# Kernel tuning notes

Hardware: AMD Instinct MI355X
Metric: run time of the kernel (lower is better)

The kernel has to match this reference:

```python
import jax, jax.numpy as jnp
import numpy as np

T, B, E = 2048, 2, 256
H = 8
D = E // H


def setup_inputs() -> dict:
    key = jax.random.key(0)
    ks = jax.random.split(key, 10)
    s = 1.0 / np.sqrt(E)
    return {
        "query": jax.random.normal(ks[0], (T, B, E), jnp.float32),
        "attn_bias": jax.random.normal(ks[1], (B, T, T), jnp.float32),
        "Wq": jax.random.normal(ks[2], (E, E), jnp.float32) * s,
        "bq": jax.random.normal(ks[3], (E,), jnp.float32) * 0.02,
        "Wk": jax.random.normal(ks[4], (E, E), jnp.float32) * s,
        "bk": jax.random.normal(ks[5], (E,), jnp.float32) * 0.02,
        "Wv": jax.random.normal(ks[6], (E, E), jnp.float32) * s,
        "bv": jax.random.normal(ks[7], (E,), jnp.float32) * 0.02,
        "Wo": jax.random.normal(ks[8], (E, E), jnp.float32) * s,
        "bo": jax.random.normal(ks[9], (E,), jnp.float32) * 0.02,
    }


def reference(query, attn_bias, Wq, bq, Wk, bk, Wv, bv, Wo, bo):
    # query: [T, B, E] (seq-first). Self-attention: k,v also projected from query.
    t, b, e = query.shape
    scaling = 1.0 / np.sqrt(D)
    q = (query @ Wq.T + bq) * scaling          # [T,B,E]
    k = query @ Wk.T + bk                      # [T,B,E]
    v = query @ Wv.T + bv                      # [T,B,E]
    q = q.reshape(t, b, H, D)
    k = k.reshape(t, b, H, D)
    v = v.reshape(t, b, H, D)
    # raw scores + per-batch additive bias broadcast across heads
    scores = jnp.einsum("tbhd,sbhd->bhts", q, k) + attn_bias[:, None, :, :]
    attn_weights = jax.nn.softmax(scores, axis=-1)  # [B,H,T,S]
    attn = jnp.einsum("bhts,sbhd->tbhd", attn_weights, v).reshape(t, b, e)
    return attn @ Wo.T + bo  # [T,B,E]
```

## Files before the change

kernel.cpp:

```cpp
#include <hip/hip_runtime.h>
#include <hip/hip_bf16.h>

#define T_DIM 2048
#define B_DIM 2
#define E_DIM 256
#define H_DIM 8
#define D_DIM 32
#define M_DIM (T_DIM*B_DIM)
#define SPLIT 4
#define S_CHUNK (T_DIM/SPLIT)
#define BHT (B_DIM*H_DIM*T_DIM)

typedef __bf16 bf16x8 __attribute__((ext_vector_type(8)));
typedef __bf16 bf16x4 __attribute__((ext_vector_type(4)));
typedef __bf16 bf16x2 __attribute__((ext_vector_type(2)));
typedef float  f32x4  __attribute__((ext_vector_type(4)));

static __device__ __forceinline__ float fexp2(float x) {
#if __has_builtin(__builtin_amdgcn_exp2f)
    return __builtin_amdgcn_exp2f(x);
#else
    return exp2f(x);
#endif
}

__global__ __launch_bounds__(256)
void qkv_kernel(const float* __restrict__ X,
                const float* __restrict__ Wq, const float* __restrict__ Wk, const float* __restrict__ Wv,
                const float* __restrict__ bq, const float* __restrict__ bk, const float* __restrict__ bv,
                __bf16* __restrict__ qh, __bf16* __restrict__ kperm, __bf16* __restrict__ vperm) {
    __shared__ __align__(16) __bf16 Xs[64][136];
    __shared__ __align__(16) __bf16 Ws[64][136];
    const int m0 = blockIdx.x * 64;
    const int which = blockIdx.y >> 2;
    const int n0 = (blockIdx.y & 3) * 64;
    const float* W = (which == 0) ? Wq : (which == 1) ? Wk : Wv;
    const float* bias = (which == 0) ? bq : (which == 1) ? bk : bv;
    const int tid = threadIdx.x;
    const int wid = tid >> 6, lane = tid & 63;
    const int wm = (wid & 1) * 32, wn = (wid >> 1) * 32;
    const int lr = lane & 15, lg = lane >> 4;

    f32x4 acc[2][2] = {};
    for (int kc = 0; kc < 2; ++kc) {
        for (int c = tid; c < 2048; c += 256) {
            int row = c >> 5, col = (c & 31) * 4;
            float4 xv = *(const float4*)&X[(size_t)(m0 + row) * E_DIM + kc * 128 + col];
            float4 wv = *(const float4*)&W[(size_t)(n0 + row) * E_DIM + kc * 128 + col];
            bf16x4 xb, wb;
            xb[0] = (__bf16)xv.x; xb[1] = (__bf16)xv.y; xb[2] = (__bf16)xv.z; xb[3] = (__bf16)xv.w;
            wb[0] = (__bf16)wv.x; wb[1] = (__bf16)wv.y; wb[2] = (__bf16)wv.z; wb[3] = (__bf16)wv.w;
            *(bf16x4*)&Xs[row][col] = xb;
            *(bf16x4*)&Ws[row][col] = wb;
        }
        __syncthreads();
#pragma unroll
        for (int ks = 0; ks < 4; ++ks) {
            bf16x8 a0 = *(const bf16x8*)&Xs[wm + lr][ks * 32 + lg * 8];
            bf16x8 a1 = *(const bf16x8*)&Xs[wm + 16 + lr][ks * 32 + lg * 8];
            bf16x8 b0 = *(const bf16x8*)&Ws[wn + lr][ks * 32 + lg * 8];
            bf16x8 b1 = *(const bf16x8*)&Ws[wn + 16 + lr][ks * 32 + lg * 8];
            acc[0][0] = __builtin_amdgcn_mfma_f32_16x16x32_bf16(a0, b0, acc[0][0], 0, 0, 0);
            acc[0][1] = __builtin_amdgcn_mfma_f32_16x16x32_bf16(a0, b1, acc[0][1], 0, 0, 0);
            acc[1][0] = __builtin_amdgcn_mfma_f32_16x16x32_bf16(a1, b0, acc[1][0], 0, 0, 0);
            acc[1][1] = __builtin_amdgcn_mfma_f32_16x16x32_bf16(a1, b1, acc[1][1], 0, 0, 0);
        }
        __syncthreads();
    }
    const float scale = 0.17677669529663687f * 1.4426950408889634f;
#pragma unroll
    for (int mt = 0; mt < 2; ++mt) {
#pragma unroll
        for (int nt = 0; nt < 2; ++nt) {
            int n = n0 + wn + nt * 16 + lr;
            float bb = bias[n];
            int h = n >> 5, d = n & 31;
#pragma unroll
            for (int r = 0; r < 4; ++r) {
                int m = m0 + wm + mt * 16 + lg * 4 + r;
                int t = m >> 1, b = m & 1;
                float v = acc[mt][nt][r] + bb;
                if (which == 0) {
                    v *= scale;
                    qh[((size_t)(b * H_DIM + h) * T_DIM + t) * D_DIM + d] = (__bf16)v;
                } else if (which == 1) {
                    int til = t >> 6, s6 = t & 63;
                    int ntk = ((s6 >> 5) << 1) | ((s6 >> 2) & 1);
                    int lrk = (((s6 >> 3) & 3) << 2) | (s6 & 3);
                    int lanek = ((d >> 3) << 4) | lrk;
                    kperm[((((size_t)(b * H_DIM + h) * 32 + til) * 4 + ntk) * 64 + lanek) * 8 + (d & 7)] = (__bf16)v;
                } else {
                    int til = t >> 6;
                    int ktv = (t >> 5) & 1, lgv = (t >> 3) & 3, elv = t & 7;
                    int jv = ktv * 2 + (d >> 4);
                    int lanev = (lgv << 4) | (d & 15);
                    vperm[((((size_t)(b * H_DIM + h) * 32 + til) * 4 + jv) * 64 + lanev) * 8 + elv] = (__bf16)v;
                }
            }
        }
    }
}

__global__ __launch_bounds__(512, 4)
void attn_kernel(const __bf16* __restrict__ qh, const __bf16* __restrict__ kperm,
                 const __bf16* __restrict__ vperm, const float* __restrict__ attn_bias,
                 __bf16* __restrict__ po, float* __restrict__ pl) {
    __shared__ __align__(16) float Bs[16][516];
    const int lin = blockIdx.x + (T_DIM / 16) * (blockIdx.y + B_DIM * blockIdx.z);
    const int combo = lin & 7;
    const int b  = combo & 1;
    const int sp = combo >> 1;
    const int t0 = (lin >> 3) * 16;
    const int tid = threadIdx.x, wid = tid >> 6, lane = tid & 63;
    const int lr = lane & 15, lg = lane >> 4;
    const int bh = b * H_DIM + wid;
    const int sbase = sp * S_CHUNK;
    const int tb0 = sp * 8;
    const float LOG2E = 1.4426950408889634f;

    {
        const float* bsrc = attn_bias + ((size_t)b * T_DIM + t0) * T_DIM + sbase;
        int r = tid >> 5, c0 = (tid & 31) * 4;
#pragma unroll
        for (int rep = 0; rep < 4; ++rep) {
            float4 v = *(const float4*)&bsrc[(size_t)r * T_DIM + rep * 128 + c0];
            float4 w;
            w.x = (v.x - 12.0f) * LOG2E;
            w.y = (v.y - 12.0f) * LOG2E;
            w.z = (v.z - 12.0f) * LOG2E;
            w.w = (v.w - 12.0f) * LOG2E;
            *(float4*)&Bs[r][rep * 128 + c0] = w;
        }
    }
    __syncthreads();

    bf16x8 qf = *(const bf16x8*)&qh[((size_t)bh * T_DIM + t0 + lr) * D_DIM + lg * 8];
    const __bf16* kpb = kperm + (size_t)bh * T_DIM * D_DIM + (size_t)lane * 8;
    const __bf16* vpb = vperm + (size_t)bh * T_DIM * D_DIM + (size_t)lane * 8;

    bf16x8 ones;
#pragma unroll
    for (int i = 0; i < 8; ++i) ones[i] = (__bf16)1.0f;

    f32x4 o0 = {}, o1 = {};
    f32x4 ol = {};

#pragma unroll
    for (int st = 0; st < 8; ++st) {
        const int til = tb0 + st;

        bf16x8 kf0 = *(const bf16x8*)&kpb[(size_t)(til * 4 + 0) * 512];
        bf16x8 kf1 = *(const bf16x8*)&kpb[(size_t)(til * 4 + 1) * 512];
        bf16x8 kf2 = *(const bf16x8*)&kpb[(size_t)(til * 4 + 2) * 512];
        bf16x8 kf3 = *(const bf16x8*)&kpb[(size_t)(til * 4 + 3) * 512];
        bf16x8 vf0 = *(const bf16x8*)&vpb[(size_t)(til * 4 + 0) * 512];
        bf16x8 vf1 = *(const bf16x8*)&vpb[(size_t)(til * 4 + 1) * 512];
        bf16x8 vf2 = *(const bf16x8*)&vpb[(size_t)(til * 4 + 2) * 512];
        bf16x8 vf3 = *(const bf16x8*)&vpb[(size_t)(til * 4 + 3) * 512];

        f32x4 cb0 = *(const f32x4*)&Bs[lr][st * 64 +  0 + lg * 8 + 0];
        f32x4 cb1 = *(const f32x4*)&Bs[lr][st * 64 +  0 + lg * 8 + 4];
        f32x4 cb2 = *(const f32x4*)&Bs[lr][st * 64 + 32 + lg * 8 + 0];
        f32x4 cb3 = *(const f32x4*)&Bs[lr][st * 64 + 32 + lg * 8 + 4];

        __builtin_amdgcn_s_setprio(1);
        f32x4 sv0 = __builtin_amdgcn_mfma_f32_16x16x32_bf16(kf0, qf, cb0, 0, 0, 0);
        f32x4 sv1 = __builtin_amdgcn_mfma_f32_16x16x32_bf16(kf1, qf, cb1, 0, 0, 0);
        f32x4 sv2 = __builtin_amdgcn_mfma_f32_16x16x32_bf16(kf2, qf, cb2, 0, 0, 0);
        f32x4 sv3 = __builtin_amdgcn_mfma_f32_16x16x32_bf16(kf3, qf, cb3, 0, 0, 0);
        __builtin_amdgcn_s_setprio(0);

        f32x4 e0, e1, e2, e3;
#pragma unroll
        for (int r = 0; r < 4; ++r) {
            e0[r] = fexp2(sv0[r]);
            e1[r] = fexp2(sv1[r]);
            e2[r] = fexp2(sv2[r]);
            e3[r] = fexp2(sv3[r]);
        }

        bf16x8 pf0, pf1;
#pragma unroll
        for (int r = 0; r < 4; ++r) {
            pf0[r] = (__bf16)e0[r]; pf0[4 + r] = (__bf16)e1[r];
            pf1[r] = (__bf16)e2[r]; pf1[4 + r] = (__bf16)e3[r];
        }

        __builtin_amdgcn_s_setprio(1);
        o0 = __builtin_amdgcn_mfma_f32_16x16x32_bf16(pf0, vf0, o0, 0, 0, 0);
        o1 = __builtin_amdgcn_mfma_f32_16x16x32_bf16(pf0, vf1, o1, 0, 0, 0);
        ol = __builtin_amdgcn_mfma_f32_16x16x32_bf16(pf0, ones, ol, 0, 0, 0);
        o0 = __builtin_amdgcn_mfma_f32_16x16x32_bf16(pf1, vf2, o0, 0, 0, 0);
        o1 = __builtin_amdgcn_mfma_f32_16x16x32_bf16(pf1, vf3, o1, 0, 0, 0);
        ol = __builtin_amdgcn_mfma_f32_16x16x32_bf16(pf1, ones, ol, 0, 0, 0);
        __builtin_amdgcn_s_setprio(0);
    }

#pragma unroll
    for (int r = 0; r < 4; ++r) {
        int t = t0 + lg * 4 + r;
        size_t rw = ((size_t)bh * T_DIM + t) * SPLIT + sp;
        bf16x2 w;
        w[0] = (__bf16)o0[r];
        w[1] = (__bf16)o1[r];
        *(bf16x2*)&po[rw * D_DIM + lr * 2] = w;
    }
    if (lr == 0)
        *(f32x4*)&pl[(size_t)sp * BHT + (size_t)bh * T_DIM + t0 + lg * 4] = ol;
}

__global__ __launch_bounds__(256)
void oproj_kernel(const __bf16* __restrict__ po, const float* __restrict__ pl,
                  const float* __restrict__ Wo, const float* __restrict__ bo,
                  float* __restrict__ out) {
    __shared__ __align__(16) __bf16 Xs[64][136];
    __shared__ __align__(16) __bf16 Ws[64][136];
    __shared__ float invLs[16][32];
    const int m0 = blockIdx.x * 64;
    const int n0 = blockIdx.y * 64;
    const int tid = threadIdx.x;
    const int wid = tid >> 6, lane = tid & 63;
    const int wm = (wid & 1) * 32, wn = (wid >> 1) * 32;
    const int lr = lane & 15, lg = lane >> 4;
    const int tb = m0 >> 1;

#pragma unroll
    for (int i = 0; i < 2; ++i) {
        int idx = tid + i * 256;
        int bhl = idx >> 5, toff = idx & 31;
        int row = bhl * T_DIM + tb + toff;
        float L = pl[row] + pl[BHT + row] + pl[2 * BHT + row] + pl[3 * BHT + row];
        invLs[bhl][toff] = 1.0f / L;
    }
    __syncthreads();

    f32x4 acc[2][2] = {};
    for (int kc = 0; kc < 2; ++kc) {
#pragma unroll
        for (int rep = 0; rep < 4; ++rep) {
            int c = tid + rep * 256;
            int m_loc = c >> 4;
            int rem = c & 15;
            int h_loc = rem >> 2, eb = rem & 3;
            int b = m_loc & 1;
            int h = kc * 4 + h_loc;
            int bh = b * H_DIM + h;
            int tl = m_loc >> 1;
            size_t row = (size_t)bh * T_DIM + tb + tl;
            const __bf16* src = po + row * (SPLIT * D_DIM) + eb * 8;
            bf16x8 v0 = *(const bf16x8*)(src);
            bf16x8 v1 = *(const bf16x8*)(src + D_DIM);
            bf16x8 v2 = *(const bf16x8*)(src + 2 * D_DIM);
            bf16x8 v3 = *(const bf16x8*)(src + 3 * D_DIM);
            float invL = invLs[bh & 15][tl];
#pragma unroll
            for (int j = 0; j < 8; ++j) {
                float s = ((float)v0[j] + (float)v1[j]) + ((float)v2[j] + (float)v3[j]);
                int d = (j & 1) * 16 + eb * 4 + (j >> 1);
                Xs[m_loc][h_loc * 32 + d] = (__bf16)(s * invL);
            }
        }
        for (int c = tid; c < 2048; c += 256) {
            int row = c >> 5, col = (c & 31) * 4;
            float4 wv = *(const float4*)&Wo[(size_t)(n0 + row) * E_DIM + kc * 128 + col];
            bf16x4 wb;
            wb[0] = (__bf16)wv.x; wb[1] = (__bf16)wv.y; wb[2] = (__bf16)wv.z; wb[3] = (__bf16)wv.w;
            *(bf16x4*)&Ws[row][col] = wb;
        }
        __syncthreads();
#pragma unroll
        for (int ks = 0; ks < 4; ++ks) {
            bf16x8 a0 = *(const bf16x8*)&Xs[wm + lr][ks * 32 + lg * 8];
            bf16x8 a1 = *(const bf16x8*)&Xs[wm + 16 + lr][ks * 32 + lg * 8];
            bf16x8 b0 = *(const bf16x8*)&Ws[wn + lr][ks * 32 + lg * 8];
            bf16x8 b1 = *(const bf16x8*)&Ws[wn + 16 + lr][ks * 32 + lg * 8];
            acc[0][0] = __builtin_amdgcn_mfma_f32_16x16x32_bf16(a0, b0, acc[0][0], 0, 0, 0);
            acc[0][1] = __builtin_amdgcn_mfma_f32_16x16x32_bf16(a0, b1, acc[0][1], 0, 0, 0);
            acc[1][0] = __builtin_amdgcn_mfma_f32_16x16x32_bf16(a1, b0, acc[1][0], 0, 0, 0);
            acc[1][1] = __builtin_amdgcn_mfma_f32_16x16x32_bf16(a1, b1, acc[1][1], 0, 0, 0);
        }
        __syncthreads();
    }
#pragma unroll
    for (int mt = 0; mt < 2; ++mt) {
#pragma unroll
        for (int nt = 0; nt < 2; ++nt) {
            int n = n0 + wn + nt * 16 + lr;
            float bb = bo[n];
#pragma unroll
            for (int r = 0; r < 4; ++r) {
                int m = m0 + wm + mt * 16 + lg * 4 + r;
                out[(size_t)m * E_DIM + n] = acc[mt][nt][r] + bb;
            }
        }
    }
}

extern "C" void kernel_launch(void* const* d_in, const int* in_sizes, int n_in,
                              void* d_out, int out_size, void* d_ws, size_t ws_size,
                              hipStream_t stream) {
    const float* query     = (const float*)d_in[0];
    const float* attn_bias = (const float*)d_in[1];
    const float* Wq = (const float*)d_in[2];
    const float* bq = (const float*)d_in[3];
    const float* Wk = (const float*)d_in[4];
    const float* bk = (const float*)d_in[5];
    const float* Wv = (const float*)d_in[6];
    const float* bv = (const float*)d_in[7];
    const float* Wo = (const float*)d_in[8];
    const float* bo = (const float*)d_in[9];
    float* out = (float*)d_out;

    char* ws = (char*)d_ws;
    __bf16* qhp  = (__bf16*)(ws);
    __bf16* kpp  = (__bf16*)(ws + 2097152);
    __bf16* vpp  = (__bf16*)(ws + 4194304);
    __bf16* po   = (__bf16*)(ws + 6291456);
    float*  pl   = (float*)(ws + 14680064);

    qkv_kernel<<<dim3(M_DIM / 64, 12), 256, 0, stream>>>(
        query, Wq, Wk, Wv, bq, bk, bv, qhp, kpp, vpp);

    attn_kernel<<<dim3(T_DIM / 16, B_DIM, SPLIT), 512, 0, stream>>>(
        qhp, kpp, vpp, attn_bias, po, pl);

    oproj_kernel<<<dim3(M_DIM / 64, E_DIM / 64), 256, 0, stream>>>(po, pl, Wo, bo, out);
}
```

Measured before the change: 53.50 us.

## Process 64 query rows per attention block to reuse K/V fragments

Each attention block now handles 64 query rows (four 16-row sub-tiles) instead of 16, so each K and V fragment loaded from global memory feeds four times as many MFMAs. The bias tile in shared memory grows to 64x516 floats (about 132 KB) and the grid shrinks by four to 256 blocks. The launch-bounds occupancy hint drops from 4 to 2, and the setprio hints are removed. The larger LDS footprint and register use cut occupancy, and fewer blocks may underfill the 256 CUs, in exchange for less redundant K/V traffic.

```diff
diff --git a/kernel.cpp b/kernel.cpp
--- a/kernel.cpp
+++ b/kernel.cpp
@@ -101,16 +101,16 @@
     }
 }
 
-__global__ __launch_bounds__(512, 4)
+__global__ __launch_bounds__(512, 2)
 void attn_kernel(const __bf16* __restrict__ qh, const __bf16* __restrict__ kperm,
                  const __bf16* __restrict__ vperm, const float* __restrict__ attn_bias,
                  __bf16* __restrict__ po, float* __restrict__ pl) {
-    __shared__ __align__(16) float Bs[16][516];
-    const int lin = blockIdx.x + (T_DIM / 16) * (blockIdx.y + B_DIM * blockIdx.z);
+    __shared__ __align__(16) float Bs[64][516];
+    const int lin = blockIdx.x + (T_DIM / 64) * (blockIdx.y + B_DIM * blockIdx.z);
     const int combo = lin & 7;
     const int b  = combo & 1;
     const int sp = combo >> 1;
-    const int t0 = (lin >> 3) * 16;
+    const int t0 = (lin >> 3) * 64;
     const int tid = threadIdx.x, wid = tid >> 6, lane = tid & 63;
     const int lr = lane & 15, lg = lane >> 4;
     const int bh = b * H_DIM + wid;
@@ -120,21 +120,25 @@
 
     {
         const float* bsrc = attn_bias + ((size_t)b * T_DIM + t0) * T_DIM + sbase;
-        int r = tid >> 5, c0 = (tid & 31) * 4;
-#pragma unroll
-        for (int rep = 0; rep < 4; ++rep) {
-            float4 v = *(const float4*)&bsrc[(size_t)r * T_DIM + rep * 128 + c0];
+#pragma unroll
+        for (int rep = 0; rep < 16; ++rep) {
+            int chunk = tid + rep * 512;
+            int row = chunk >> 7, col = (chunk & 127) * 4;
+            float4 v = *(const float4*)&bsrc[(size_t)row * T_DIM + col];
             float4 w;
             w.x = (v.x - 12.0f) * LOG2E;
             w.y = (v.y - 12.0f) * LOG2E;
             w.z = (v.z - 12.0f) * LOG2E;
             w.w = (v.w - 12.0f) * LOG2E;
-            *(float4*)&Bs[r][rep * 128 + c0] = w;
+            *(float4*)&Bs[row][col] = w;
         }
     }
     __syncthreads();
 
-    bf16x8 qf = *(const bf16x8*)&qh[((size_t)bh * T_DIM + t0 + lr) * D_DIM + lg * 8];
+    bf16x8 qf[4];
+#pragma unroll
+    for (int sub = 0; sub < 4; ++sub)
+        qf[sub] = *(const bf16x8*)&qh[((size_t)bh * T_DIM + t0 + sub * 16 + lr) * D_DIM + lg * 8];
     const __bf16* kpb = kperm + (size_t)bh * T_DIM * D_DIM + (size_t)lane * 8;
     const __bf16* vpb = vperm + (size_t)bh * T_DIM * D_DIM + (size_t)lane * 8;
 
@@ -142,8 +146,7 @@
 #pragma unroll
     for (int i = 0; i < 8; ++i) ones[i] = (__bf16)1.0f;
 
-    f32x4 o0 = {}, o1 = {};
-    f32x4 ol = {};
+    f32x4 o0[4] = {}, o1[4] = {}, ol[4] = {};
 
 #pragma unroll
     for (int st = 0; st < 8; ++st) {
@@ -158,55 +161,57 @@
         bf16x8 vf2 = *(const bf16x8*)&vpb[(size_t)(til * 4 + 2) * 512];
         bf16x8 vf3 = *(const bf16x8*)&vpb[(size_t)(til * 4 + 3) * 512];
 
-        f32x4 cb0 = *(const f32x4*)&Bs[lr][st * 64 +  0 + lg * 8 + 0];
-        f32x4 cb1 = *(const f32x4*)&Bs[lr][st * 64 +  0 + lg * 8 + 4];
-        f32x4 cb2 = *(const f32x4*)&Bs[lr][st * 64 + 32 + lg * 8 + 0];
-        f32x4 cb3 = *(const f32x4*)&Bs[lr][st * 64 + 32 + lg * 8 + 4];
-
-        __builtin_amdgcn_s_setprio(1);
-        f32x4 sv0 = __builtin_amdgcn_mfma_f32_16x16x32_bf16(kf0, qf, cb0, 0, 0, 0);
-        f32x4 sv1 = __builtin_amdgcn_mfma_f32_16x16x32_bf16(kf1, qf, cb1, 0, 0, 0);
-        f32x4 sv2 = __builtin_amdgcn_mfma_f32_16x16x32_bf16(kf2, qf, cb2, 0, 0, 0);
-        f32x4 sv3 = __builtin_amdgcn_mfma_f32_16x16x32_bf16(kf3, qf, cb3, 0, 0, 0);
-        __builtin_amdgcn_s_setprio(0);
-
-        f32x4 e0, e1, e2, e3;
+#pragma unroll
+        for (int sub = 0; sub < 4; ++sub) {
+            f32x4 cb0 = *(const f32x4*)&Bs[sub * 16 + lr][st * 64 +  0 + lg * 8 + 0];
+            f32x4 cb1 = *(const f32x4*)&Bs[sub * 16 + lr][st * 64 +  0 + lg * 8 + 4];
+            f32x4 cb2 = *(const f32x4*)&Bs[sub * 16 + lr][st * 64 + 32 + lg * 8 + 0];
+            f32x4 cb3 = *(const f32x4*)&Bs[sub * 16 + lr][st * 64 + 32 + lg * 8 + 4];
+
+            f32x4 sv0 = __builtin_amdgcn_mfma_f32_16x16x32_bf16(kf0, qf[sub], cb0, 0, 0, 0);
+            f32x4 sv1 = __builtin_amdgcn_mfma_f32_16x16x32_bf16(kf1, qf[sub], cb1, 0, 0, 0);
+            f32x4 sv2 = __builtin_amdgcn_mfma_f32_16x16x32_bf16(kf2, qf[sub], cb2, 0, 0, 0);
+            f32x4 sv3 = __builtin_amdgcn_mfma_f32_16x16x32_bf16(kf3, qf[sub], cb3, 0, 0, 0);
+
+            f32x4 e0, e1, e2, e3;
+#pragma unroll
+            for (int r = 0; r < 4; ++r) {
+                e0[r] = fexp2(sv0[r]);
+                e1[r] = fexp2(sv1[r]);
+                e2[r] = fexp2(sv2[r]);
+                e3[r] = fexp2(sv3[r]);
+            }
+
+            bf16x8 pf0, pf1;
+#pragma unroll
+            for (int r = 0; r < 4; ++r) {
+                pf0[r] = (__bf16)e0[r]; pf0[4 + r] = (__bf16)e1[r];
+                pf1[r] = (__bf16)e2[r]; pf1[4 + r] = (__bf16)e3[r];
+            }
+
+            o0[sub] = __builtin_amdgcn_mfma_f32_16x16x32_bf16(pf0, vf0, o0[sub], 0, 0, 0);
+            o1[sub] = __builtin_amdgcn_mfma_f32_16x16x32_bf16(pf0, vf1, o1[sub], 0, 0, 0);
+            ol[sub] = __builtin_amdgcn_mfma_f32_16x16x32_bf16(pf0, ones, ol[sub], 0, 0, 0);
+            o0[sub] = __builtin_amdgcn_mfma_f32_16x16x32_bf16(pf1, vf2, o0[sub], 0, 0, 0);
+            o1[sub] = __builtin_amdgcn_mfma_f32_16x16x32_bf16(pf1, vf3, o1[sub], 0, 0, 0);
+            ol[sub] = __builtin_amdgcn_mfma_f32_16x16x32_bf16(pf1, ones, ol[sub], 0, 0, 0);
+        }
+    }
+
+#pragma unroll
+    for (int sub = 0; sub < 4; ++sub) {
 #pragma unroll
         for (int r = 0; r < 4; ++r) {
-            e0[r] = fexp2(sv0[r]);
-            e1[r] = fexp2(sv1[r]);
-            e2[r] = fexp2(sv2[r]);
-            e3[r] = fexp2(sv3[r]);
-        }
-
-        bf16x8 pf0, pf1;
-#pragma unroll
-        for (int r = 0; r < 4; ++r) {
-            pf0[r] = (__bf16)e0[r]; pf0[4 + r] = (__bf16)e1[r];
-            pf1[r] = (__bf16)e2[r]; pf1[4 + r] = (__bf16)e3[r];
-        }
-
-        __builtin_amdgcn_s_setprio(1);
-        o0 = __builtin_amdgcn_mfma_f32_16x16x32_bf16(pf0, vf0, o0, 0, 0, 0);
-        o1 = __builtin_amdgcn_mfma_f32_16x16x32_bf16(pf0, vf1, o1, 0, 0, 0);
-        ol = __builtin_amdgcn_mfma_f32_16x16x32_bf16(pf0, ones, ol, 0, 0, 0);
-        o0 = __builtin_amdgcn_mfma_f32_16x16x32_bf16(pf1, vf2, o0, 0, 0, 0);
-        o1 = __builtin_amdgcn_mfma_f32_16x16x32_bf16(pf1, vf3, o1, 0, 0, 0);
-        ol = __builtin_amdgcn_mfma_f32_16x16x32_bf16(pf1, ones, ol, 0, 0, 0);
-        __builtin_amdgcn_s_setprio(0);
-    }
-
-#pragma unroll
-    for (int r = 0; r < 4; ++r) {
-        int t = t0 + lg * 4 + r;
-        size_t rw = ((size_t)bh * T_DIM + t) * SPLIT + sp;
-        bf16x2 w;
-        w[0] = (__bf16)o0[r];
-        w[1] = (__bf16)o1[r];
-        *(bf16x2*)&po[rw * D_DIM + lr * 2] = w;
-    }
-    if (lr == 0)
-        *(f32x4*)&pl[(size_t)sp * BHT + (size_t)bh * T_DIM + t0 + lg * 4] = ol;
+            int t = t0 + sub * 16 + lg * 4 + r;
+            size_t rw = ((size_t)bh * T_DIM + t) * SPLIT + sp;
+            bf16x2 w;
+            w[0] = (__bf16)o0[sub][r];
+            w[1] = (__bf16)o1[sub][r];
+            *(bf16x2*)&po[rw * D_DIM + lr * 2] = w;
+        }
+        if (lr == 0)
+            *(f32x4*)&pl[(size_t)sp * BHT + (size_t)bh * T_DIM + t0 + sub * 16 + lg * 4] = ol[sub];
+    }
 }
 
 __global__ __launch_bounds__(256)
@@ -321,7 +326,7 @@
     qkv_kernel<<<dim3(M_DIM / 64, 12), 256, 0, stream>>>(
         query, Wq, Wk, Wv, bq, bk, bv, qhp, kpp, vpp);
 
-    attn_kernel<<<dim3(T_DIM / 16, B_DIM, SPLIT), 512, 0, stream>>>(
+    attn_kernel<<<dim3(T_DIM / 64, B_DIM, SPLIT), 512, 0, stream>>>(
         qhp, kpp, vpp, attn_bias, po, pl);
 
     oproj_kernel<<<dim3(M_DIM / 64, E_DIM / 64), 256, 0, stream>>>(po, pl, Wo, bo, out);
```

Result: faster. 49.29 us (-7.9%).

## Drop split-S attention, stage QKV permuted stores through LDS, normalize in attention

Applied to the files above, without the earlier changes.

The attention kernel no longer splits the key dimension four ways. Each block now processes the full 2048-key range with the whole 16x2048 bias tile in LDS, and each wave starts at a staggered tile offset. Output is normalized inside the attention kernel, so the output-projection kernel no longer reads four partial outputs and row sums. The QKV kernel now writes its permuted bf16 outputs through an LDS buffer with coalesced 16-byte stores, and the s_setprio hints are removed. The trade-off is fewer blocks (256 vs 1024) with a large LDS footprint (~131KB) that limits occupancy, in exchange for less partial-sum traffic and less reduction work.

```diff
diff --git a/kernel.cpp b/kernel.cpp
--- a/kernel.cpp
+++ b/kernel.cpp
@@ -7,9 +7,6 @@
 #define H_DIM 8
 #define D_DIM 32
 #define M_DIM (T_DIM*B_DIM)
-#define SPLIT 4
-#define S_CHUNK (T_DIM/SPLIT)
-#define BHT (B_DIM*H_DIM*T_DIM)
 
 typedef __bf16 bf16x8 __attribute__((ext_vector_type(8)));
 typedef __bf16 bf16x4 __attribute__((ext_vector_type(4)));
@@ -31,6 +28,7 @@
                 __bf16* __restrict__ qh, __bf16* __restrict__ kperm, __bf16* __restrict__ vperm) {
     __shared__ __align__(16) __bf16 Xs[64][136];
     __shared__ __align__(16) __bf16 Ws[64][136];
+    __shared__ __align__(16) __bf16 Ps[4][1024];
     const int m0 = blockIdx.x * 64;
     const int which = blockIdx.y >> 2;
     const int n0 = (blockIdx.y & 3) * 64;
@@ -68,68 +66,84 @@
         __syncthreads();
     }
     const float scale = 0.17677669529663687f * 1.4426950408889634f;
+    const int tb = m0 >> 1;
+    const int hl0 = n0 >> 5;
+
 #pragma unroll
     for (int mt = 0; mt < 2; ++mt) {
 #pragma unroll
         for (int nt = 0; nt < 2; ++nt) {
             int n = n0 + wn + nt * 16 + lr;
             float bb = bias[n];
-            int h = n >> 5, d = n & 31;
+            int hl = (n >> 5) - hl0, d = n & 31;
 #pragma unroll
             for (int r = 0; r < 4; ++r) {
                 int m = m0 + wm + mt * 16 + lg * 4 + r;
-                int t = m >> 1, b = m & 1;
+                int tt = (m >> 1) - tb, b = m & 1;
                 float v = acc[mt][nt][r] + bb;
+                int off;
                 if (which == 0) {
                     v *= scale;
-                    qh[((size_t)(b * H_DIM + h) * T_DIM + t) * D_DIM + d] = (__bf16)v;
+                    off = tt * 32 + d;
                 } else if (which == 1) {
-                    int til = t >> 6, s6 = t & 63;
-                    int ntk = ((s6 >> 5) << 1) | ((s6 >> 2) & 1);
-                    int lrk = (((s6 >> 3) & 3) << 2) | (s6 & 3);
-                    int lanek = ((d >> 3) << 4) | lrk;
-                    kperm[((((size_t)(b * H_DIM + h) * 32 + til) * 4 + ntk) * 64 + lanek) * 8 + (d & 7)] = (__bf16)v;
+                    off = ((tt >> 2) & 1) * 512 +
+                          ((((d >> 3) << 4) | (((tt >> 3) & 3) << 2) | (tt & 3)) << 3) + (d & 7);
                 } else {
-                    int til = t >> 6;
-                    int ktv = (t >> 5) & 1, lgv = (t >> 3) & 3, elv = t & 7;
-                    int jv = ktv * 2 + (d >> 4);
-                    int lanev = (lgv << 4) | (d & 15);
-                    vperm[((((size_t)(b * H_DIM + h) * 32 + til) * 4 + jv) * 64 + lanev) * 8 + elv] = (__bf16)v;
+                    off = (d >> 4) * 512 +
+                          (((((tt >> 3) & 3) << 4) | (d & 15)) << 3) + (tt & 7);
                 }
+                Ps[b * 2 + hl][off] = (__bf16)v;
             }
         }
+    }
+    __syncthreads();
+
+    {
+        int combo = tid >> 6, e0 = (tid & 63) * 16;
+        int bc = combo >> 1, hl = combo & 1;
+        int bh = bc * H_DIM + hl0 + hl;
+        int til = tb >> 6;
+        __bf16* dst;
+        if (which == 0) {
+            dst = qh + ((size_t)bh * T_DIM + tb) * D_DIM;
+        } else if (which == 1) {
+            int ntk0 = ((tb >> 5) & 1) << 1;
+            dst = kperm + (((size_t)bh * 32 + til) * 4 + ntk0) * 512;
+        } else {
+            int ktv = (tb >> 5) & 1;
+            dst = vperm + (((size_t)bh * 32 + til) * 4 + ktv * 2) * 512;
+        }
+        *(bf16x8*)(dst + e0)     = *(const bf16x8*)&Ps[combo][e0];
+        *(bf16x8*)(dst + e0 + 8) = *(const bf16x8*)&Ps[combo][e0 + 8];
     }
 }
 
 __global__ __launch_bounds__(512, 4)
 void attn_kernel(const __bf16* __restrict__ qh, const __bf16* __restrict__ kperm,
                  const __bf16* __restrict__ vperm, const float* __restrict__ attn_bias,
-                 __bf16* __restrict__ po, float* __restrict__ pl) {
-    __shared__ __align__(16) float Bs[16][516];
-    const int lin = blockIdx.x + (T_DIM / 16) * (blockIdx.y + B_DIM * blockIdx.z);
-    const int combo = lin & 7;
-    const int b  = combo & 1;
-    const int sp = combo >> 1;
-    const int t0 = (lin >> 3) * 16;
+                 __bf16* __restrict__ att) {
+    __shared__ __align__(16) float Bs[16][2052];
+    const int lin = blockIdx.x;
+    const int b  = lin & 1;
+    const int t0 = (lin >> 1) * 16;
     const int tid = threadIdx.x, wid = tid >> 6, lane = tid & 63;
     const int lr = lane & 15, lg = lane >> 4;
     const int bh = b * H_DIM + wid;
-    const int sbase = sp * S_CHUNK;
-    const int tb0 = sp * 8;
     const float LOG2E = 1.4426950408889634f;
 
     {
-        const float* bsrc = attn_bias + ((size_t)b * T_DIM + t0) * T_DIM + sbase;
-        int r = tid >> 5, c0 = (tid & 31) * 4;
-#pragma unroll
-        for (int rep = 0; rep < 4; ++rep) {
-            float4 v = *(const float4*)&bsrc[(size_t)r * T_DIM + rep * 128 + c0];
+        const float* bsrc = attn_bias + ((size_t)b * T_DIM + t0) * T_DIM;
+#pragma unroll
+        for (int rep = 0; rep < 16; ++rep) {
+            int c = tid + rep * 512;
+            int row = c >> 9, col = (c & 511) * 4;
+            float4 v = *(const float4*)&bsrc[(size_t)row * T_DIM + col];
             float4 w;
             w.x = (v.x - 12.0f) * LOG2E;
             w.y = (v.y - 12.0f) * LOG2E;
             w.z = (v.z - 12.0f) * LOG2E;
             w.w = (v.w - 12.0f) * LOG2E;
-            *(float4*)&Bs[r][rep * 128 + c0] = w;
+            *(float4*)&Bs[row][col] = w;
         }
     }
     __syncthreads();
@@ -145,9 +159,9 @@
     f32x4 o0 = {}, o1 = {};
     f32x4 ol = {};
 
-#pragma unroll
-    for (int st = 0; st < 8; ++st) {
-        const int til = tb0 + st;
+#pragma unroll 4
+    for (int st = 0; st < 32; ++st) {
+        const int til = (st + wid * 4) & 31;
 
         bf16x8 kf0 = *(const bf16x8*)&kpb[(size_t)(til * 4 + 0) * 512];
         bf16x8 kf1 = *(const bf16x8*)&kpb[(size_t)(til * 4 + 1) * 512];
@@ -158,17 +172,15 @@
         bf16x8 vf2 = *(const bf16x8*)&vpb[(size_t)(til * 4 + 2) * 512];
         bf16x8 vf3 = *(const bf16x8*)&vpb[(size_t)(til * 4 + 3) * 512];
 
-        f32x4 cb0 = *(const f32x4*)&Bs[lr][st * 64 +  0 + lg * 8 + 0];
-        f32x4 cb1 = *(const f32x4*)&Bs[lr][st * 64 +  0 + lg * 8 + 4];
-        f32x4 cb2 = *(const f32x4*)&Bs[lr][st * 64 + 32 + lg * 8 + 0];
-        f32x4 cb3 = *(const f32x4*)&Bs[lr][st * 64 + 32 + lg * 8 + 4];
-
-        __builtin_amdgcn_s_setprio(1);
+        f32x4 cb0 = *(const f32x4*)&Bs[lr][til * 64 +  0 + lg * 8 + 0];
+        f32x4 cb1 = *(const f32x4*)&Bs[lr][til * 64 +  0 + lg * 8 + 4];
+        f32x4 cb2 = *(const f32x4*)&Bs[lr][til * 64 + 32 + lg * 8 + 0];
+        f32x4 cb3 = *(const f32x4*)&Bs[lr][til * 64 + 32 + lg * 8 + 4];
+
         f32x4 sv0 = __builtin_amdgcn_mfma_f32_16x16x32_bf16(kf0, qf, cb0, 0, 0, 0);
         f32x4 sv1 = __builtin_amdgcn_mfma_f32_16x16x32_bf16(kf1, qf, cb1, 0, 0, 0);
         f32x4 sv2 = __builtin_amdgcn_mfma_f32_16x16x32_bf16(kf2, qf, cb2, 0, 0, 0);
         f32x4 sv3 = __builtin_amdgcn_mfma_f32_16x16x32_bf16(kf3, qf, cb3, 0, 0, 0);
-        __builtin_amdgcn_s_setprio(0);
 
         f32x4 e0, e1, e2, e3;
 #pragma unroll
@@ -186,36 +198,31 @@
             pf1[r] = (__bf16)e2[r]; pf1[4 + r] = (__bf16)e3[r];
         }
 
-        __builtin_amdgcn_s_setprio(1);
         o0 = __builtin_amdgcn_mfma_f32_16x16x32_bf16(pf0, vf0, o0, 0, 0, 0);
         o1 = __builtin_amdgcn_mfma_f32_16x16x32_bf16(pf0, vf1, o1, 0, 0, 0);
         ol = __builtin_amdgcn_mfma_f32_16x16x32_bf16(pf0, ones, ol, 0, 0, 0);
         o0 = __builtin_amdgcn_mfma_f32_16x16x32_bf16(pf1, vf2, o0, 0, 0, 0);
         o1 = __builtin_amdgcn_mfma_f32_16x16x32_bf16(pf1, vf3, o1, 0, 0, 0);
         ol = __builtin_amdgcn_mfma_f32_16x16x32_bf16(pf1, ones, ol, 0, 0, 0);
-        __builtin_amdgcn_s_setprio(0);
     }
 
 #pragma unroll
     for (int r = 0; r < 4; ++r) {
         int t = t0 + lg * 4 + r;
-        size_t rw = ((size_t)bh * T_DIM + t) * SPLIT + sp;
+        float inv = 1.0f / ol[r];
         bf16x2 w;
-        w[0] = (__bf16)o0[r];
-        w[1] = (__bf16)o1[r];
-        *(bf16x2*)&po[rw * D_DIM + lr * 2] = w;
-    }
-    if (lr == 0)
-        *(f32x4*)&pl[(size_t)sp * BHT + (size_t)bh * T_DIM + t0 + lg * 4] = ol;
+        w[0] = (__bf16)(o0[r] * inv);
+        w[1] = (__bf16)(o1[r] * inv);
+        *(bf16x2*)&att[((size_t)bh * T_DIM + t) * D_DIM + lr * 2] = w;
+    }
 }
 
 __global__ __launch_bounds__(256)
-void oproj_kernel(const __bf16* __restrict__ po, const float* __restrict__ pl,
+void oproj_kernel(const __bf16* __restrict__ att,
                   const float* __restrict__ Wo, const float* __restrict__ bo,
                   float* __restrict__ out) {
     __shared__ __align__(16) __bf16 Xs[64][136];
     __shared__ __align__(16) __bf16 Ws[64][136];
-    __shared__ float invLs[16][32];
     const int m0 = blockIdx.x * 64;
     const int n0 = blockIdx.y * 64;
     const int tid = threadIdx.x;
@@ -223,16 +230,6 @@
     const int wm = (wid & 1) * 32, wn = (wid >> 1) * 32;
     const int lr = lane & 15, lg = lane >> 4;
     const int tb = m0 >> 1;
-
-#pragma unroll
-    for (int i = 0; i < 2; ++i) {
-        int idx = tid + i * 256;
-        int bhl = idx >> 5, toff = idx & 31;
-        int row = bhl * T_DIM + tb + toff;
-        float L = pl[row] + pl[BHT + row] + pl[2 * BHT + row] + pl[3 * BHT + row];
-        invLs[bhl][toff] = 1.0f / L;
-    }
-    __syncthreads();
 
     f32x4 acc[2][2] = {};
     for (int kc = 0; kc < 2; ++kc) {
@@ -247,17 +244,11 @@
             int bh = b * H_DIM + h;
             int tl = m_loc >> 1;
             size_t row = (size_t)bh * T_DIM + tb + tl;
-            const __bf16* src = po + row * (SPLIT * D_DIM) + eb * 8;
-            bf16x8 v0 = *(const bf16x8*)(src);
-            bf16x8 v1 = *(const bf16x8*)(src + D_DIM);
-            bf16x8 v2 = *(const bf16x8*)(src + 2 * D_DIM);
-            bf16x8 v3 = *(const bf16x8*)(src + 3 * D_DIM);
-            float invL = invLs[bh & 15][tl];
+            bf16x8 v = *(const bf16x8*)&att[row * D_DIM + eb * 8];
 #pragma unroll
             for (int j = 0; j < 8; ++j) {
-                float s = ((float)v0[j] + (float)v1[j]) + ((float)v2[j] + (float)v3[j]);
                 int d = (j & 1) * 16 + eb * 4 + (j >> 1);
-                Xs[m_loc][h_loc * 32 + d] = (__bf16)(s * invL);
+                Xs[m_loc][h_loc * 32 + d] = v[j];
             }
         }
         for (int c = tid; c < 2048; c += 256) {
@@ -315,14 +306,13 @@
     __bf16* qhp  = (__bf16*)(ws);
     __bf16* kpp  = (__bf16*)(ws + 2097152);
     __bf16* vpp  = (__bf16*)(ws + 4194304);
-    __bf16* po   = (__bf16*)(ws + 6291456);
-    float*  pl   = (float*)(ws + 14680064);
+    __bf16* att  = (__bf16*)(ws + 6291456);
 
     qkv_kernel<<<dim3(M_DIM / 64, 12), 256, 0, stream>>>(
         query, Wq, Wk, Wv, bq, bk, bv, qhp, kpp, vpp);
 
-    attn_kernel<<<dim3(T_DIM / 16, B_DIM, SPLIT), 512, 0, stream>>>(
-        qhp, kpp, vpp, attn_bias, po, pl);
-
-    oproj_kernel<<<dim3(M_DIM / 64, E_DIM / 64), 256, 0, stream>>>(po, pl, Wo, bo, out);
-}
+    attn_kernel<<<dim3((T_DIM / 16) * B_DIM), 512, 0, stream>>>(
+        qhp, kpp, vpp, attn_bias, att);
+
+    oproj_kernel<<<dim3(M_DIM / 64, E_DIM / 64), 256, 0, stream>>>(att, Wo, bo, out);
+}
```

Result: faster. 51.29 us (-4.1%).
